# Kernel optimization log

Measured on AMD Instinct MI355X. Metric: run time of the kernel, lower is better.

The kernel has to match this reference:

```python
import jax, jax.numpy as jnp
import numpy as np

N = 50000        # nodes
E = 800000       # edges
H = 128          # in = hidden = out width
L = 4            # num_layers
BN_EPS = 1e-5


def _bn(x, g, b):
    # training-mode batch norm over the node dimension (biased variance, as torch)
    mu = jnp.mean(x, axis=0)
    var = jnp.mean((x - mu) ** 2, axis=0)
    return (x - mu) * jax.lax.rsqrt(var + BN_EPS) * g + b


def setup_inputs() -> dict:
    key = jax.random.key(0)
    ks = jax.random.split(key, 16)
    s = 0.05
    return {
        "x": jax.random.normal(ks[0], (N, H), dtype=jnp.float32),
        "edge_index": jax.random.randint(ks[1], (2, E), 0, N, dtype=jnp.int32),
        # stacked per-layer MLP params (all layers share dims H->H->H)
        "fc1_w": jax.random.normal(ks[2], (L, H, H), dtype=jnp.float32) * s,
        "fc1_b": jnp.zeros((L, H), dtype=jnp.float32),
        "bn1_g": jnp.ones((L, H), dtype=jnp.float32),
        "bn1_b": jnp.zeros((L, H), dtype=jnp.float32),
        "fc2_w": jax.random.normal(ks[3], (L, H, H), dtype=jnp.float32) * s,
        "fc2_b": jnp.zeros((L, H), dtype=jnp.float32),
        "bn2_g": jnp.ones((L, H), dtype=jnp.float32),
        "bn2_b": jnp.zeros((L, H), dtype=jnp.float32),
        # outer per-layer BatchNorm (intended one-per-GIN-layer)
        "bn3_g": jnp.ones((L, H), dtype=jnp.float32),
        "bn3_b": jnp.zeros((L, H), dtype=jnp.float32),
        # final classifier
        "fc_w": jax.random.normal(ks[4], (H, H), dtype=jnp.float32) * s,
        "fc_b": jnp.zeros((H,), dtype=jnp.float32),
    }


def reference(x, edge_index, fc1_w, fc1_b, bn1_g, bn1_b, fc2_w, fc2_b,
              bn2_g, bn2_b, bn3_g, bn3_b, fc_w, fc_b):
    src = edge_index[0]
    dst = edge_index[1]
    for i in range(L):
        # GINConv, eps=0: h = MLP((1+eps)*x + sum_{j in N(v)} x_j)
        agg = jax.ops.segment_sum(x[src], dst, num_segments=N)  # [N, H]
        h = x + agg
        # MLP: relu(bn1(fc1(h))) -> bn2(fc2(.))
        h = jax.nn.relu(_bn(h @ fc1_w[i].T + fc1_b[i], bn1_g[i], bn1_b[i]))
        h = _bn(h @ fc2_w[i].T + fc2_b[i], bn2_g[i], bn2_b[i])
        # outer BN + ReLU per layer
        x = jax.nn.relu(_bn(h, bn3_g[i], bn3_b[i]))
    return x @ fc_w.T + fc_b  # [N, H]
```

## Files before the change

kernel.cpp:

```cpp
#include <hip/hip_runtime.h>
#include <hip/hip_bf16.h>

#define NN 50000
#define HD 128
#define NL 4
#define BN_EPS 1e-5f
#define NTILES 3125

typedef __attribute__((ext_vector_type(8))) short short8;
typedef __attribute__((ext_vector_type(4))) float f32x4;

__device__ inline ushort f2bf(float f){
  uint u = __float_as_uint(f);
  uint r = (u + 0x7fffu + ((u >> 16) & 1u)) >> 16;
  return (ushort)r;
}
__device__ inline float bflo(uint u){ return __uint_as_float(u << 16); }
__device__ inline float bfhi(uint u){ return __uint_as_float(u & 0xffff0000u); }

__global__ void cast_f32_bf16x4(const float* __restrict__ in, ushort* __restrict__ out, int n4){
  int i = blockIdx.x * blockDim.x + threadIdx.x;
  int stride = gridDim.x * blockDim.x;
  const float4* in4 = (const float4*)in;
  for (; i < n4; i += stride){
    float4 v = in4[i];
    ushort4 r;
    r.x = f2bf(v.x); r.y = f2bf(v.y); r.z = f2bf(v.z); r.w = f2bf(v.w);
    *(ushort4*)(out + i * 4) = r;
  }
}

__global__ void cast_weights(const float* __restrict__ w1, const float* __restrict__ w2,
                             const float* __restrict__ wf, ushort* __restrict__ wb){
  int i = blockIdx.x * 256 + threadIdx.x;
  if (i >= 36864) return;
  const float* src;
  if (i < 16384)      src = w1 + i * 4;
  else if (i < 32768) src = w2 + (i - 16384) * 4;
  else                src = wf + (i - 32768) * 4;
  float4 v = *(const float4*)src;
  ushort4 r;
  r.x = f2bf(v.x); r.y = f2bf(v.y); r.z = f2bf(v.z); r.w = f2bf(v.w);
  *(ushort4*)(wb + i * 4) = r;
}

__global__ void fill1_kernel(const int* __restrict__ dst, int* __restrict__ cnt,
                             int* __restrict__ pos, int E){
  int e = (blockIdx.x * 256 + threadIdx.x) * 4;
  if (e + 4 <= E){
    int4 d = *(const int4*)(dst + e);
    int4 p;
    p.x = atomicAdd(&cnt[d.x], 1);
    p.y = atomicAdd(&cnt[d.y], 1);
    p.z = atomicAdd(&cnt[d.z], 1);
    p.w = atomicAdd(&cnt[d.w], 1);
    *(int4*)(pos + e) = p;
  } else {
    for (; e < E; ++e) pos[e] = atomicAdd(&cnt[dst[e]], 1);
  }
}

__global__ void scan1_kernel(const int* __restrict__ deg, int* __restrict__ incl,
                             int* __restrict__ bsum, int n){
  __shared__ int tmp[1024];
  int gid = blockIdx.x * 1024 + threadIdx.x;
  int v = (gid < n) ? deg[gid] : 0;
  tmp[threadIdx.x] = v;
  __syncthreads();
  for (int ofs = 1; ofs < 1024; ofs <<= 1){
    int t = tmp[threadIdx.x];
    int a = (threadIdx.x >= ofs) ? tmp[threadIdx.x - ofs] : 0;
    __syncthreads();
    tmp[threadIdx.x] = t + a;
    __syncthreads();
  }
  if (gid < n) incl[gid] = tmp[threadIdx.x];
  if (threadIdx.x == 1023) bsum[blockIdx.x] = tmp[1023];
}

__global__ void scan2_kernel(const int* __restrict__ bsum, int* __restrict__ base,
                             int* __restrict__ off, int nb, int n){
  if (threadIdx.x == 0){
    int run = 0;
    for (int i = 0; i < nb; ++i){ base[i] = run; run += bsum[i]; }
    off[n] = run;
  }
}

__global__ void scan3_kernel(const int* __restrict__ deg, const int* __restrict__ incl,
                             const int* __restrict__ base, int* __restrict__ off, int n){
  int gid = blockIdx.x * 1024 + threadIdx.x;
  if (gid < n) off[gid] = incl[gid] - deg[gid] + base[blockIdx.x];
}

__global__ void fill2_kernel(const int* __restrict__ src, const int* __restrict__ dst,
                             const int* __restrict__ off, const int* __restrict__ pos,
                             int* __restrict__ csrc, int E){
  int e = (blockIdx.x * 256 + threadIdx.x) * 4;
  if (e + 4 <= E){
    int4 d = *(const int4*)(dst + e);
    int4 p = *(const int4*)(pos + e);
    int4 s = *(const int4*)(src + e);
    csrc[off[d.x] + p.x] = s.x;
    csrc[off[d.y] + p.y] = s.y;
    csrc[off[d.z] + p.z] = s.z;
    csrc[off[d.w] + p.w] = s.w;
  } else {
    for (; e < E; ++e) csrc[off[dst[e]] + pos[e]] = src[e];
  }
}

__device__ inline void bn_params_tid(const float* st, const float* gA, const float* gB,
                                     const float* bB, int mode, float* sS, float* sT){
  int c = threadIdx.x;
  if (c < 128){
    const float invN = 1.f / (float)NN;
    float mu = st[c] * invN;
    float var = fmaxf(st[128 + c] * invN - mu * mu, 0.f);
    float S, T;
    if (mode == 0){
      S = gA[c] * rsqrtf(var + BN_EPS);
      T = gB[c] - mu * S;
    } else {
      float inv2 = rsqrtf(var + BN_EPS);
      float tt = gA[c] * inv2;
      float inv3 = rsqrtf(tt * tt * var + BN_EPS);
      S = tt * inv3 * gB[c];
      T = bB[c] - mu * S;
    }
    sS[c] = S; sT[c] = T;
  }
}

__global__ __launch_bounds__(256) void agg_kernel(const ushort* __restrict__ xb,
                                                  const int* __restrict__ off,
                                                  const int* __restrict__ csrc,
                                                  ushort* __restrict__ h){
  int node = blockIdx.x * 4 + (threadIdx.x >> 6);
  int lane = threadIdx.x & 63;
  const uint* xr = (const uint*)xb;
  uint self = xr[node * 64 + lane];
  float ax = bflo(self), ay = bfhi(self);
  int s = off[node], e = off[node + 1];
  int j = s;
  for (; j + 8 <= e; j += 8){
    uint v0 = xr[csrc[j+0]*64+lane], v1 = xr[csrc[j+1]*64+lane];
    uint v2 = xr[csrc[j+2]*64+lane], v3 = xr[csrc[j+3]*64+lane];
    uint v4 = xr[csrc[j+4]*64+lane], v5 = xr[csrc[j+5]*64+lane];
    uint v6 = xr[csrc[j+6]*64+lane], v7 = xr[csrc[j+7]*64+lane];
    ax += bflo(v0)+bflo(v1)+bflo(v2)+bflo(v3)+bflo(v4)+bflo(v5)+bflo(v6)+bflo(v7);
    ay += bfhi(v0)+bfhi(v1)+bfhi(v2)+bfhi(v3)+bfhi(v4)+bfhi(v5)+bfhi(v6)+bfhi(v7);
  }
  for (; j + 4 <= e; j += 4){
    uint v0 = xr[csrc[j+0]*64+lane], v1 = xr[csrc[j+1]*64+lane];
    uint v2 = xr[csrc[j+2]*64+lane], v3 = xr[csrc[j+3]*64+lane];
    ax += bflo(v0)+bflo(v1)+bflo(v2)+bflo(v3);
    ay += bfhi(v0)+bfhi(v1)+bfhi(v2)+bfhi(v3);
  }
  for (; j < e; ++j){
    uint v = xr[csrc[j] * 64 + lane];
    ax += bflo(v); ay += bfhi(v);
  }
  uint o = (uint)f2bf(ax) | ((uint)f2bf(ay) << 16);
  ((uint*)h)[node * 64 + lane] = o;
}

__global__ __launch_bounds__(256) void agg_bn_kernel(const ushort* __restrict__ yb,
                                                     const int* __restrict__ off,
                                                     const int* __restrict__ csrc,
                                                     const float* __restrict__ statsIn,
                                                     const float* __restrict__ g2,
                                                     const float* __restrict__ g3,
                                                     const float* __restrict__ b3,
                                                     ushort* __restrict__ h){
  __shared__ float sS[128];
  __shared__ float sT[128];
  bn_params_tid(statsIn, g2, g3, b3, 1, sS, sT);
  __syncthreads();
  int node = blockIdx.x * 4 + (threadIdx.x >> 6);
  int lane = threadIdx.x & 63;
  float S0 = sS[lane*2], T0 = sT[lane*2];
  float S1 = sS[lane*2+1], T1 = sT[lane*2+1];
  const uint* xr = (const uint*)yb;
  uint self = xr[node * 64 + lane];
  float ax = fmaxf(bflo(self)*S0+T0, 0.f), ay = fmaxf(bfhi(self)*S1+T1, 0.f);
  int s = off[node], e = off[node + 1];
  int j = s;
  for (; j + 4 <= e; j += 4){
    uint v0 = xr[csrc[j+0]*64+lane], v1 = xr[csrc[j+1]*64+lane];
    uint v2 = xr[csrc[j+2]*64+lane], v3 = xr[csrc[j+3]*64+lane];
    ax += fmaxf(bflo(v0)*S0+T0,0.f) + fmaxf(bflo(v1)*S0+T0,0.f)
        + fmaxf(bflo(v2)*S0+T0,0.f) + fmaxf(bflo(v3)*S0+T0,0.f);
    ay += fmaxf(bfhi(v0)*S1+T1,0.f) + fmaxf(bfhi(v1)*S1+T1,0.f)
        + fmaxf(bfhi(v2)*S1+T1,0.f) + fmaxf(bfhi(v3)*S1+T1,0.f);
  }
  for (; j < e; ++j){
    uint v = xr[csrc[j] * 64 + lane];
    ax += fmaxf(bflo(v)*S0+T0,0.f);
    ay += fmaxf(bfhi(v)*S1+T1,0.f);
  }
  uint o = (uint)f2bf(ax) | ((uint)f2bf(ay) << 16);
  ((uint*)h)[node * 64 + lane] = o;
}

__global__ __launch_bounds__(512) void gemm_kernel(const ushort* __restrict__ A,
                                                   const ushort* __restrict__ W,
                                                   const float* __restrict__ bias,
                                                   ushort* __restrict__ Yb,
                                                   float* __restrict__ Yf,
                                                   float* __restrict__ statsOut,
                                                   const float* __restrict__ statsIn,
                                                   const float* __restrict__ gA,
                                                   const float* __restrict__ gB,
                                                   const float* __restrict__ bB,
                                                   int mode){
  __shared__ uint4 w4[128 * 17];
  __shared__ float ssum[128];
  __shared__ float ssq[128];
  __shared__ float sS[128];
  __shared__ float sT[128];
  const uint4* Wg = (const uint4*)W;
  for (int c = threadIdx.x; c < 2048; c += 512){
    w4[(c >> 4) * 17 + (c & 15)] = Wg[c];
  }
  if (statsIn) bn_params_tid(statsIn, gA, gB, bB, mode, sS, sT);
  if (threadIdx.x < 128){ ssum[threadIdx.x] = 0.f; ssq[threadIdx.x] = 0.f; }
  __syncthreads();

  int wave = threadIdx.x >> 6;
  int lane = threadIdx.x & 63;
  int m = lane & 15, q = lane >> 4;
  int tile = blockIdx.x * 8 + wave;
  bool tv = tile < NTILES;
  const uint4* A4 = (const uint4*)A;

  f32x4 acc[8];
#pragma unroll
  for (int i = 0; i < 8; ++i) acc[i] = (f32x4)0.f;

#pragma unroll
  for (int kt = 0; kt < 4; ++kt){
    short8 af = (short8)0;
    if (tv){
      uint4 t = A4[(tile * 16 + m) * 16 + kt * 4 + q];
      if (statsIn){
        int kc = kt * 32 + q * 8;
        uint4 pk;
        pk.x = (uint)f2bf(fmaxf(bflo(t.x)*sS[kc+0]+sT[kc+0],0.f))
             | ((uint)f2bf(fmaxf(bfhi(t.x)*sS[kc+1]+sT[kc+1],0.f)) << 16);
        pk.y = (uint)f2bf(fmaxf(bflo(t.y)*sS[kc+2]+sT[kc+2],0.f))
             | ((uint)f2bf(fmaxf(bfhi(t.y)*sS[kc+3]+sT[kc+3],0.f)) << 16);
        pk.z = (uint)f2bf(fmaxf(bflo(t.z)*sS[kc+4]+sT[kc+4],0.f))
             | ((uint)f2bf(fmaxf(bfhi(t.z)*sS[kc+5]+sT[kc+5],0.f)) << 16);
        pk.w = (uint)f2bf(fmaxf(bflo(t.w)*sS[kc+6]+sT[kc+6],0.f))
             | ((uint)f2bf(fmaxf(bfhi(t.w)*sS[kc+7]+sT[kc+7],0.f)) << 16);
        t = pk;
      }
      af = *(short8*)&t;
    }
#pragma unroll
    for (int to = 0; to < 8; ++to){
      uint4 bw = w4[(to * 16 + m) * 17 + kt * 4 + q];
      acc[to] = __builtin_amdgcn_mfma_f32_16x16x32_bf16(af, *(short8*)&bw, acc[to], 0, 0, 0);
    }
  }

  bool dost = (statsOut != nullptr);
#pragma unroll
  for (int to = 0; to < 8; ++to){
    int col = to * 16 + m;
    float bc = bias[col];
    float ls = 0.f, lq = 0.f;
    if (tv){
#pragma unroll
      for (int r = 0; r < 4; ++r){
        float v = acc[to][r] + bc;
        int row = tile * 16 + q * 4 + r;
        if (Yb) Yb[row * 128 + col] = __builtin_bit_cast(ushort, f2bf(v));
        else    Yf[row * 128 + col] = v;
        ls += v; lq += v * v;
      }
    }
    if (dost){
      ls += __shfl_xor(ls, 16); lq += __shfl_xor(lq, 16);
      ls += __shfl_xor(ls, 32); lq += __shfl_xor(lq, 32);
      if (tv && q == 0){ atomicAdd(&ssum[col], ls); atomicAdd(&ssq[col], lq); }
    }
  }
  if (dost){
    __syncthreads();
    if (threadIdx.x < 128){
      atomicAdd(&statsOut[threadIdx.x], ssum[threadIdx.x]);
      atomicAdd(&statsOut[128 + threadIdx.x], ssq[threadIdx.x]);
    }
  }
}

extern "C" void kernel_launch(void* const* d_in, const int* in_sizes, int n_in,
                              void* d_out, int out_size, void* d_ws, size_t ws_size,
                              hipStream_t stream) {
  const float* x     = (const float*)d_in[0];
  const int*   ei    = (const int*)d_in[1];
  const float* fc1_w = (const float*)d_in[2];
  const float* fc1_b = (const float*)d_in[3];
  const float* bn1_g = (const float*)d_in[4];
  const float* bn1_b = (const float*)d_in[5];
  const float* fc2_w = (const float*)d_in[6];
  const float* fc2_b = (const float*)d_in[7];
  const float* bn2_g = (const float*)d_in[8];
  const float* bn3_g = (const float*)d_in[10];
  const float* bn3_b = (const float*)d_in[11];
  const float* fc_w  = (const float*)d_in[12];
  const float* fc_b  = (const float*)d_in[13];

  int E = in_sizes[1] / 2;
  const int* srcp = ei;
  const int* dstp = ei + E;

  char* ws = (char*)d_ws;
  int*    off    = (int*)(ws + 0);
  int*    cnt    = (int*)(ws + 200064);
  int*    pos    = (int*)(ws + 400128);
  int*    csrc   = (int*)(ws + 3600128);
  ushort* wb     = (ushort*)(ws + 6800128);
  float*  stats  = (float*)(ws + 7095040);
  int*    sscr   = (int*)(ws + 7103232);
  ushort* xb     = (ushort*)(ws + 7104256);
  ushort* hb     = (ushort*)(ws + 19904256);
  ushort* y1b    = (ushort*)(ws + 32704256);
  ushort* y2b    = (ushort*)(ws + 45504256);

  int* incl = csrc;
  int* bsum = sscr;
  int* base = sscr + 64;

  hipMemsetAsync(cnt, 0, 200064, stream);
  hipMemsetAsync(stats, 0, 8192, stream);

  cast_f32_bf16x4<<<2048, 256, 0, stream>>>(x, xb, NN * HD / 4);
  cast_weights<<<144, 256, 0, stream>>>(fc1_w, fc2_w, fc_w, wb);

  const int EB4 = (E / 4 + 255) / 256 + 1;
  const int SB = (NN + 1023) / 1024;
  fill1_kernel<<<EB4, 256, 0, stream>>>(dstp, cnt, pos, E);
  scan1_kernel<<<SB, 1024, 0, stream>>>(cnt, incl, bsum, NN);
  scan2_kernel<<<1, 64, 0, stream>>>(bsum, base, off, SB, NN);
  scan3_kernel<<<SB, 1024, 0, stream>>>(cnt, incl, base, off, NN);
  fill2_kernel<<<EB4, 256, 0, stream>>>(srcp, dstp, off, pos, csrc, E);

  const int gb = (NTILES + 7) / 8;

  for (int i = 0; i < NL; ++i){
    if (i == 0){
      agg_kernel<<<NN / 4, 256, 0, stream>>>(xb, off, csrc, hb);
    } else {
      agg_bn_kernel<<<NN / 4, 256, 0, stream>>>(y2b, off, csrc,
                                                stats + (i - 1) * 512 + 256,
                                                bn2_g + (i - 1) * 128,
                                                bn3_g + (i - 1) * 128,
                                                bn3_b + (i - 1) * 128, hb);
    }
    gemm_kernel<<<gb, 512, 0, stream>>>(hb, wb + i * 16384, fc1_b + i * 128,
                                        y1b, nullptr, stats + i * 512,
                                        nullptr, nullptr, nullptr, nullptr, 0);
    gemm_kernel<<<gb, 512, 0, stream>>>(y1b, wb + 65536 + i * 16384, fc2_b + i * 128,
                                        y2b, nullptr, stats + i * 512 + 256,
                                        stats + i * 512, bn1_g + i * 128,
                                        bn1_b + i * 128, nullptr, 0);
  }

  gemm_kernel<<<gb, 512, 0, stream>>>(y2b, wb + 131072, fc_b,
                                      nullptr, (float*)d_out, nullptr,
                                      stats + 3 * 512 + 256, bn2_g + 384,
                                      bn3_g + 384, bn3_b + 384, 1);
}
```

Measured before the change: 487.4 us.

## Precompute BN+ReLU activations once and gather with 16-byte vector loads

```diff
diff --git a/kernel.cpp b/kernel.cpp
--- a/kernel.cpp
+++ b/kernel.cpp
@@ -17,6 +17,9 @@
 }
 __device__ inline float bflo(uint u){ return __uint_as_float(u << 16); }
 __device__ inline float bfhi(uint u){ return __uint_as_float(u & 0xffff0000u); }
+__device__ inline uint pk2(float lo, float hi){
+  return (uint)f2bf(lo) | ((uint)f2bf(hi) << 16);
+}
 
 __global__ void cast_f32_bf16x4(const float* __restrict__ in, ushort* __restrict__ out, int n4){
   int i = blockIdx.x * blockDim.x + threadIdx.x;
@@ -80,11 +83,16 @@
 
 __global__ void scan2_kernel(const int* __restrict__ bsum, int* __restrict__ base,
                              int* __restrict__ off, int nb, int n){
-  if (threadIdx.x == 0){
-    int run = 0;
-    for (int i = 0; i < nb; ++i){ base[i] = run; run += bsum[i]; }
-    off[n] = run;
-  }
+  int lane = threadIdx.x & 63;
+  int own = (lane < nb) ? bsum[lane] : 0;
+  int v = own;
+#pragma unroll
+  for (int ofs = 1; ofs < 64; ofs <<= 1){
+    int t = __shfl_up(v, ofs);
+    if (lane >= ofs) v += t;
+  }
+  if (lane < nb) base[lane] = v - own;
+  if (lane == 63) off[n] = v;
 }
 
 __global__ void scan3_kernel(const int* __restrict__ deg, const int* __restrict__ incl,
@@ -132,75 +140,89 @@
   }
 }
 
+__global__ __launch_bounds__(256) void xform_kernel(const ushort* __restrict__ y,
+                                                    const float* __restrict__ statsIn,
+                                                    const float* __restrict__ g2,
+                                                    const float* __restrict__ g3,
+                                                    const float* __restrict__ b3,
+                                                    ushort* __restrict__ xo){
+  __shared__ float sS[128];
+  __shared__ float sT[128];
+  bn_params_tid(statsIn, g2, g3, b3, 1, sS, sT);
+  __syncthreads();
+  int i0 = blockIdx.x * 256 + threadIdx.x;
+  int cb = (i0 & 15) * 8;
+  float S[8], T[8];
+#pragma unroll
+  for (int k = 0; k < 8; ++k){ S[k] = sS[cb + k]; T[k] = sT[cb + k]; }
+  const uint4* y4 = (const uint4*)y;
+  uint4* o4 = (uint4*)xo;
+  const int total = NN * 16;
+  int stride = gridDim.x * 256;
+  for (int i = i0; i < total; i += stride){
+    uint4 v = y4[i];
+    uint4 r;
+    r.x = pk2(fmaxf(bflo(v.x)*S[0]+T[0],0.f), fmaxf(bfhi(v.x)*S[1]+T[1],0.f));
+    r.y = pk2(fmaxf(bflo(v.y)*S[2]+T[2],0.f), fmaxf(bfhi(v.y)*S[3]+T[3],0.f));
+    r.z = pk2(fmaxf(bflo(v.z)*S[4]+T[4],0.f), fmaxf(bfhi(v.z)*S[5]+T[5],0.f));
+    r.w = pk2(fmaxf(bflo(v.w)*S[6]+T[6],0.f), fmaxf(bfhi(v.w)*S[7]+T[7],0.f));
+    o4[i] = r;
+  }
+}
+
 __global__ __launch_bounds__(256) void agg_kernel(const ushort* __restrict__ xb,
                                                   const int* __restrict__ off,
                                                   const int* __restrict__ csrc,
                                                   ushort* __restrict__ h){
-  int node = blockIdx.x * 4 + (threadIdx.x >> 6);
+  const uint4* x4 = (const uint4*)xb;
+  uint4* h4 = (uint4*)h;
   int lane = threadIdx.x & 63;
-  const uint* xr = (const uint*)xb;
-  uint self = xr[node * 64 + lane];
-  float ax = bflo(self), ay = bfhi(self);
-  int s = off[node], e = off[node + 1];
-  int j = s;
-  for (; j + 8 <= e; j += 8){
-    uint v0 = xr[csrc[j+0]*64+lane], v1 = xr[csrc[j+1]*64+lane];
-    uint v2 = xr[csrc[j+2]*64+lane], v3 = xr[csrc[j+3]*64+lane];
-    uint v4 = xr[csrc[j+4]*64+lane], v5 = xr[csrc[j+5]*64+lane];
-    uint v6 = xr[csrc[j+6]*64+lane], v7 = xr[csrc[j+7]*64+lane];
-    ax += bflo(v0)+bflo(v1)+bflo(v2)+bflo(v3)+bflo(v4)+bflo(v5)+bflo(v6)+bflo(v7);
-    ay += bfhi(v0)+bfhi(v1)+bfhi(v2)+bfhi(v3)+bfhi(v4)+bfhi(v5)+bfhi(v6)+bfhi(v7);
-  }
-  for (; j + 4 <= e; j += 4){
-    uint v0 = xr[csrc[j+0]*64+lane], v1 = xr[csrc[j+1]*64+lane];
-    uint v2 = xr[csrc[j+2]*64+lane], v3 = xr[csrc[j+3]*64+lane];
-    ax += bflo(v0)+bflo(v1)+bflo(v2)+bflo(v3);
-    ay += bfhi(v0)+bfhi(v1)+bfhi(v2)+bfhi(v3);
-  }
-  for (; j < e; ++j){
-    uint v = xr[csrc[j] * 64 + lane];
-    ax += bflo(v); ay += bfhi(v);
-  }
-  uint o = (uint)f2bf(ax) | ((uint)f2bf(ay) << 16);
-  ((uint*)h)[node * 64 + lane] = o;
-}
-
-__global__ __launch_bounds__(256) void agg_bn_kernel(const ushort* __restrict__ yb,
-                                                     const int* __restrict__ off,
-                                                     const int* __restrict__ csrc,
-                                                     const float* __restrict__ statsIn,
-                                                     const float* __restrict__ g2,
-                                                     const float* __restrict__ g3,
-                                                     const float* __restrict__ b3,
-                                                     ushort* __restrict__ h){
-  __shared__ float sS[128];
-  __shared__ float sT[128];
-  bn_params_tid(statsIn, g2, g3, b3, 1, sS, sT);
-  __syncthreads();
-  int node = blockIdx.x * 4 + (threadIdx.x >> 6);
-  int lane = threadIdx.x & 63;
-  float S0 = sS[lane*2], T0 = sT[lane*2];
-  float S1 = sS[lane*2+1], T1 = sT[lane*2+1];
-  const uint* xr = (const uint*)yb;
-  uint self = xr[node * 64 + lane];
-  float ax = fmaxf(bflo(self)*S0+T0, 0.f), ay = fmaxf(bfhi(self)*S1+T1, 0.f);
-  int s = off[node], e = off[node + 1];
-  int j = s;
-  for (; j + 4 <= e; j += 4){
-    uint v0 = xr[csrc[j+0]*64+lane], v1 = xr[csrc[j+1]*64+lane];
-    uint v2 = xr[csrc[j+2]*64+lane], v3 = xr[csrc[j+3]*64+lane];
-    ax += fmaxf(bflo(v0)*S0+T0,0.f) + fmaxf(bflo(v1)*S0+T0,0.f)
-        + fmaxf(bflo(v2)*S0+T0,0.f) + fmaxf(bflo(v3)*S0+T0,0.f);
-    ay += fmaxf(bfhi(v0)*S1+T1,0.f) + fmaxf(bfhi(v1)*S1+T1,0.f)
-        + fmaxf(bfhi(v2)*S1+T1,0.f) + fmaxf(bfhi(v3)*S1+T1,0.f);
-  }
-  for (; j < e; ++j){
-    uint v = xr[csrc[j] * 64 + lane];
-    ax += fmaxf(bflo(v)*S0+T0,0.f);
-    ay += fmaxf(bfhi(v)*S1+T1,0.f);
-  }
-  uint o = (uint)f2bf(ax) | ((uint)f2bf(ay) << 16);
-  ((uint*)h)[node * 64 + lane] = o;
+  int grp  = lane >> 4;
+  int col  = lane & 15;
+  for (int node = blockIdx.x * 4 + (threadIdx.x >> 6); node < NN; node += gridDim.x * 4){
+    int s = off[node], e = off[node + 1];
+    float a0, a1, a2, a3, a4, a5, a6, a7;
+    if (grp == 0){
+      uint4 v = x4[node * 16 + col];
+      a0 = bflo(v.x); a1 = bfhi(v.x); a2 = bflo(v.y); a3 = bfhi(v.y);
+      a4 = bflo(v.z); a5 = bfhi(v.z); a6 = bflo(v.w); a7 = bfhi(v.w);
+    } else {
+      a0=0.f;a1=0.f;a2=0.f;a3=0.f;a4=0.f;a5=0.f;a6=0.f;a7=0.f;
+    }
+    int j = s + grp;
+    while (j + 4 < e){
+      int r0 = csrc[j];
+      int r1 = csrc[j + 4];
+      uint4 v0 = x4[r0 * 16 + col];
+      uint4 v1 = x4[r1 * 16 + col];
+      a0 += bflo(v0.x) + bflo(v1.x); a1 += bfhi(v0.x) + bfhi(v1.x);
+      a2 += bflo(v0.y) + bflo(v1.y); a3 += bfhi(v0.y) + bfhi(v1.y);
+      a4 += bflo(v0.z) + bflo(v1.z); a5 += bfhi(v0.z) + bfhi(v1.z);
+      a6 += bflo(v0.w) + bflo(v1.w); a7 += bfhi(v0.w) + bfhi(v1.w);
+      j += 8;
+    }
+    if (j < e){
+      uint4 v = x4[csrc[j] * 16 + col];
+      a0 += bflo(v.x); a1 += bfhi(v.x);
+      a2 += bflo(v.y); a3 += bfhi(v.y);
+      a4 += bflo(v.z); a5 += bfhi(v.z);
+      a6 += bflo(v.w); a7 += bfhi(v.w);
+    }
+    a0 += __shfl_xor(a0, 16); a1 += __shfl_xor(a1, 16);
+    a2 += __shfl_xor(a2, 16); a3 += __shfl_xor(a3, 16);
+    a4 += __shfl_xor(a4, 16); a5 += __shfl_xor(a5, 16);
+    a6 += __shfl_xor(a6, 16); a7 += __shfl_xor(a7, 16);
+    a0 += __shfl_xor(a0, 32); a1 += __shfl_xor(a1, 32);
+    a2 += __shfl_xor(a2, 32); a3 += __shfl_xor(a3, 32);
+    a4 += __shfl_xor(a4, 32); a5 += __shfl_xor(a5, 32);
+    a6 += __shfl_xor(a6, 32); a7 += __shfl_xor(a7, 32);
+    if (grp == 0){
+      uint4 o;
+      o.x = pk2(a0, a1); o.y = pk2(a2, a3);
+      o.z = pk2(a4, a5); o.w = pk2(a6, a7);
+      h4[node * 16 + col] = o;
+    }
+  }
 }
 
 __global__ __launch_bounds__(512) void gemm_kernel(const ushort* __restrict__ A,
@@ -351,15 +373,7 @@
   const int gb = (NTILES + 7) / 8;
 
   for (int i = 0; i < NL; ++i){
-    if (i == 0){
-      agg_kernel<<<NN / 4, 256, 0, stream>>>(xb, off, csrc, hb);
-    } else {
-      agg_bn_kernel<<<NN / 4, 256, 0, stream>>>(y2b, off, csrc,
-                                                stats + (i - 1) * 512 + 256,
-                                                bn2_g + (i - 1) * 128,
-                                                bn3_g + (i - 1) * 128,
-                                                bn3_b + (i - 1) * 128, hb);
-    }
+    agg_kernel<<<2048, 256, 0, stream>>>(xb, off, csrc, hb);
     gemm_kernel<<<gb, 512, 0, stream>>>(hb, wb + i * 16384, fc1_b + i * 128,
                                         y1b, nullptr, stats + i * 512,
                                         nullptr, nullptr, nullptr, nullptr, 0);
@@ -367,6 +381,11 @@
                                         y2b, nullptr, stats + i * 512 + 256,
                                         stats + i * 512, bn1_g + i * 128,
                                         bn1_b + i * 128, nullptr, 0);
+    if (i < NL - 1){
+      xform_kernel<<<1024, 256, 0, stream>>>(y2b, stats + i * 512 + 256,
+                                             bn2_g + i * 128, bn3_g + i * 128,
+                                             bn3_b + i * 128, xb);
+    }
   }
 
   gemm_kernel<<<gb, 512, 0, stream>>>(y2b, wb + 131072, fc_b,
```

Measured after the change: 472.1 us. 1.03x faster.
